# Performance work log

Hardware: AMD Instinct MI355X
Metric: run time of the kernel (lower is better)

## Reference

```python
import jax, jax.numpy as jnp
import numpy as np

NUM_LEVELS = 4
RADIUS = 4


def _avg_pool2(x):
    # F.avg_pool2d(x, 2, stride=2) for even H, W
    B, D, H, W = x.shape
    return x.reshape(B, D, H // 2, 2, W // 2, 2).mean(axis=(3, 5))


def _local_corr(f1, f2, coords, radius):
    # f1, f2: (B, D, H, W); coords: (B, 2, H, W) pixel coords into f2
    B, D, H, W = f1.shape
    offs = jnp.arange(-radius, radius + 1, dtype=coords.dtype)
    dx, dy = jnp.meshgrid(offs, offs, indexing='ij')  # x slow, y fast (as in _get_local_grids)
    dx = dx.reshape(-1)
    dy = dy.reshape(-1)  # (K,) with K=(2r+1)^2
    x = coords[:, 0][..., None] + dx  # (B,H,W,K)
    y = coords[:, 1][..., None] + dy
    # grid_sample(padding_mode='border', align_corners=True) == clamp coords then bilinear
    x = jnp.clip(x, 0.0, W - 1.0)
    y = jnp.clip(y, 0.0, H - 1.0)
    x0 = jnp.floor(x)
    y0 = jnp.floor(y)
    x1 = jnp.minimum(x0 + 1.0, W - 1.0)
    y1 = jnp.minimum(y0 + 1.0, H - 1.0)
    wx1 = x - x0
    wx0 = 1.0 - wx1
    wy1 = y - y0
    wy0 = 1.0 - wy1
    f2f = f2.reshape(B, D, H * W)

    def corner(xc, yc, w):
        idx = (yc * W + xc).astype(jnp.int32).reshape(B, -1)  # (B, H*W*K)
        g = jax.vmap(lambda f, i: jnp.take(f, i, axis=1))(f2f, idx)  # (B,D,H*W*K)
        g = g.reshape(B, D, H, W, -1)  # (B,D,H,W,K)
        # per-pixel dot over feature dim, weighted by bilinear weight
        return w * jnp.einsum('bdhw,bdhwk->bhwk', f1, g)

    corr = (corner(x0, y0, wx0 * wy0) + corner(x1, y0, wx1 * wy0)
            + corner(x0, y1, wx0 * wy1) + corner(x1, y1, wx1 * wy1))
    corr = corr / jnp.sqrt(jnp.asarray(D, dtype=corr.dtype))
    return jnp.transpose(corr, (0, 3, 1, 2))  # (B,K,H,W)


def _corr_pyramid(fmap1, fmap2, coords):
    p1, p2 = [fmap1], [fmap2]
    for _ in range(NUM_LEVELS - 1):
        p1.append(_avg_pool2(p1[-1]))
        p2.append(_avg_pool2(p2[-1]))
    outs = []
    B = coords.shape[0]
    for i in range(NUM_LEVELS):
        Hl, Wl = p1[i].shape[2], p1[i].shape[3]
        if i == 0:
            c = coords
        else:
            c = jax.image.resize(coords, (B, 2, Hl, Wl), method='linear')
        c = c / (2.0 ** i)  # coords / scale, per level
        outs.append(_local_corr(p1[i], p2[i], c, RADIUS))
    return tuple(outs)


def setup_inputs() -> dict:
    key = jax.random.key(0)
    k1, k2, k3 = jax.random.split(key, 3)
    B, D, H, W = 1, 128, 64, 96
    fmap1 = jax.random.normal(k1, (B, D, H, W), dtype=jnp.float32)
    fmap2 = jax.random.normal(k2, (B, D, H, W), dtype=jnp.float32)
    yy, xx = jnp.meshgrid(jnp.arange(H, dtype=jnp.float32),
                          jnp.arange(W, dtype=jnp.float32), indexing='ij')
    base = jnp.stack([xx, yy], axis=0)[None]  # (1,2,H,W), coords_grid order (x,y)
    flow = 3.0 * jax.random.normal(k3, (B, 2, H, W), dtype=jnp.float32)
    coords = base + flow
    return {"fmap1": fmap1, "fmap2": fmap2, "coords": coords}


def reference(fmap1, fmap2, coords):
    return _corr_pyramid(fmap1, fmap2, coords)
```

## Files before the change

kernel.cpp:

```cpp
#include <hip/hip_runtime.h>
#include <hip/hip_fp16.h>

#define D 128
#define H0 64
#define W0 96
#define HW0 6144
#define INV_SQRT_D 0.08838834764831843f

#define H_F1T0 0
#define H_F1T1 786432
#define H_F1T2 983040
#define H_F1T3 1032192
#define H_F2T0 1048576
#define H_F2T1 1835008
#define H_F2T2 2031616
#define H_F2T3 2080768

#define OUT_L0 0
#define OUT_L1 497664
#define OUT_L2 622080
#define OUT_L3 653184

typedef _Float16 h2 __attribute__((ext_vector_type(2)));
union F4H { float4 f; h2 h[4]; };

__device__ __forceinline__ float dot2f(h2 a, h2 b, float c) {
#if __has_builtin(__builtin_amdgcn_fdot2)
    return __builtin_amdgcn_fdot2(a, b, c, false);
#else
    return c + (float)a.x * (float)b.x + (float)a.y * (float)b.y;
#endif
}

__device__ __forceinline__ void gp_to_level(int gp, int& level, int& p) {
    if (gp < 6144)      { level = 0; p = gp; }
    else if (gp < 7680) { level = 1; p = gp - 6144; }
    else if (gp < 8064) { level = 2; p = gp - 7680; }
    else                { level = 3; p = gp - 8064; }
}

__global__ __launch_bounds__(256) void k_prep(const float* __restrict__ f1,
                                              const float* __restrict__ f2,
                                              float* __restrict__ ws) {
    const int b = blockIdx.x;
    const int t = threadIdx.x;
    _Float16* wh = (_Float16*)ws;
    __shared__ float T[64 * 69];
    const int m = b / 192;
    const int rb = b - m * 192;
    const int tix = rb >> 1;
    const int dh = rb & 1;
    const int tr = tix / 12, tc = tix - (tix / 12) * 12;
    const float* in = (m ? f2 : f1) + dh * 64 * HW0;

    const int l = t & 63;
    const int gbase = (tr * 8 + (l >> 3)) * W0 + tc * 8 + (l & 7);
#pragma unroll 4
    for (int pass = 0; pass < 16; ++pass) {
        int d = pass * 4 + (t >> 6);
        T[l * 69 + d] = in[d * HW0 + gbase];
    }
    __syncthreads();

    _Float16* o0 = wh + (m ? H_F2T0 : H_F1T0) + dh * 64;
#pragma unroll 4
    for (int pass = 0; pass < 16; ++pass) {
        int e = t + pass * 256;
        int pl = e >> 6, c = e & 63;
        int gp = (tr * 8 + (pl >> 3)) * W0 + tc * 8 + (pl & 7);
        o0[gp * D + c] = (_Float16)T[pl * 69 + c];
    }
    _Float16* o1 = wh + (m ? H_F2T1 : H_F1T1) + dh * 64;
#pragma unroll
    for (int pass = 0; pass < 4; ++pass) {
        int e = t + pass * 256;
        int d = e & 63, p1 = e >> 6;
        int i1 = p1 >> 2, j1 = p1 & 3;
        int l00 = (i1 * 2) * 8 + j1 * 2;
        float v = T[l00 * 69 + d] + T[(l00 + 1) * 69 + d]
                + T[(l00 + 8) * 69 + d] + T[(l00 + 9) * 69 + d];
        o1[((tr * 4 + i1) * 48 + tc * 4 + j1) * D + d] = (_Float16)(0.25f * v);
    }
    _Float16* o2 = wh + (m ? H_F2T2 : H_F1T2) + dh * 64;
    {
        int d = t & 63, p2 = t >> 6;
        int i2 = p2 >> 1, j2 = p2 & 1;
        float acc = 0.0f;
#pragma unroll
        for (int a = 0; a < 4; ++a)
#pragma unroll
            for (int c2 = 0; c2 < 4; ++c2)
                acc += T[((i2 * 4 + a) * 8 + j2 * 4 + c2) * 69 + d];
        o2[((tr * 2 + i2) * 24 + tc * 2 + j2) * D + d] = (_Float16)(acc * 0.0625f);
    }
    _Float16* o3 = wh + (m ? H_F2T3 : H_F1T3) + dh * 64;
    if (t < 64) {
        float acc = 0.0f;
        for (int l2 = 0; l2 < 64; ++l2) acc += T[l2 * 69 + t];
        o3[(tr * 12 + tc) * D + t] = (_Float16)(acc * 0.015625f);
    }
}

__global__ __launch_bounds__(1024) void k_dc(const float* __restrict__ coords0,
                                             const float* __restrict__ ws,
                                             float* __restrict__ out) {
    __shared__ float Gs[16 * 101];
    __shared__ float cxs[16], cys[16];
    const _Float16* wh = (const _Float16*)ws;

    const int t = threadIdx.x;
    const int w = t >> 6;
    const int ln = t & 63;
    const int oct = ln >> 3;
    const int sub = ln & 7;

    const int gp0 = blockIdx.x * 16;
    const int gp = gp0 + w;

    int level, p;
    gp_to_level(gp, level, p);
    const int Hl = H0 >> level, Wl = W0 >> level;

    const int f1offs[4] = {H_F1T0, H_F1T1, H_F1T2, H_F1T3};
    const int f2offs[4] = {H_F2T0, H_F2T1, H_F2T2, H_F2T3};
    const int outoffs[4] = {OUT_L0, OUT_L1, OUT_L2, OUT_L3};

    const _Float16* f2t = wh + f2offs[level];

    float cx, cy;
    if (level == 0) {
        cx = coords0[p];
        cy = coords0[HW0 + p];
    } else {
        const int ho = p / Wl, wo = p - (p / Wl) * Wl;
        const float ff = (float)(1 << level);
        const float sfy = (ho + 0.5f) * ff - 0.5f;
        const float sfx = (wo + 0.5f) * ff - 0.5f;
        int ylo = max(0, (int)ceilf(sfy - ff));
        int yhi = min(H0 - 1, (int)floorf(sfy + ff));
        int xlo = max(0, (int)ceilf(sfx - ff));
        int xhi = min(W0 - 1, (int)floorf(sfx + ff));
        int nx = xhi - xlo + 1;
        int nt = (yhi - ylo + 1) * nx;
        float a0 = 0.0f, a1 = 0.0f, wsum = 0.0f;
        for (int i = ln; i < nt; i += 64) {
            int ry = i / nx, rx = i - ry * nx;
            int iy = ylo + ry, ix = xlo + rx;
            float wy = fmaxf(1.0f - fabsf(sfy - (float)iy) / ff, 0.0f);
            float wx = fmaxf(1.0f - fabsf(sfx - (float)ix) / ff, 0.0f);
            float wgt = wy * wx;
            wsum += wgt;
            a0 += wgt * coords0[iy * W0 + ix];
            a1 += wgt * coords0[HW0 + iy * W0 + ix];
        }
#pragma unroll
        for (int off = 32; off; off >>= 1) {
            a0 += __shfl_xor(a0, off);
            a1 += __shfl_xor(a1, off);
            wsum += __shfl_xor(wsum, off);
        }
        cx = a0 / wsum / ff;
        cy = a1 / wsum / ff;
    }
    if (ln == 0) { cxs[w] = cx; cys[w] = cy; }
    const int fx = (int)floorf(cx), fy = (int)floorf(cy);

    const _Float16* f1p = wh + f1offs[level] + p * D + sub * 8;
    F4H a0f, a1f;
    a0f.f = *(const float4*)(f1p);
    a1f.f = *(const float4*)(f1p + 64);

#pragma unroll 2
    for (int i = 0; i < 13; ++i) {
        int g = i * 8 + oct;
        int gc = min(g, 99);
        int gy = gc / 10;
        int gx = gc - gy * 10;
        int iy = min(max(fy - 4 + gy, 0), Hl - 1);
        int ix = min(max(fx - 4 + gx, 0), Wl - 1);
        const _Float16* row = f2t + (iy * Wl + ix) * D + sub * 8;
        F4H v0, v1;
        v0.f = *(const float4*)(row);
        v1.f = *(const float4*)(row + 64);
        float s = 0.0f;
        s = dot2f(a0f.h[0], v0.h[0], s);
        s = dot2f(a0f.h[1], v0.h[1], s);
        s = dot2f(a0f.h[2], v0.h[2], s);
        s = dot2f(a0f.h[3], v0.h[3], s);
        s = dot2f(a1f.h[0], v1.h[0], s);
        s = dot2f(a1f.h[1], v1.h[1], s);
        s = dot2f(a1f.h[2], v1.h[2], s);
        s = dot2f(a1f.h[3], v1.h[3], s);
        s += __shfl_xor(s, 1);
        s += __shfl_xor(s, 2);
        s += __shfl_xor(s, 4);
        if (sub == 0 && g < 100) Gs[w * 101 + g] = s;
    }
    __syncthreads();

    {
        const int px = t & 15;
        const int kk = t >> 4;
        int lv0, p0;
        gp_to_level(gp0, lv0, p0);
        const int Hb = H0 >> lv0, Wb = W0 >> lv0;
        const int npb = Hb * Wb;
        float* outp = out + outoffs[lv0] + p0 + px;
        const float bx = cxs[px], by = cys[px];
        const float Wm1 = (float)(Wb - 1), Hm1 = (float)(Hb - 1);
        const float* Gp = &Gs[px * 101];

        for (int k = kk; k < 81; k += 64) {
            int dxi = k / 9, dyi = k - (k / 9) * 9;
            float x = fminf(fmaxf(bx + (float)(dxi - 4), 0.0f), Wm1);
            float y = fminf(fmaxf(by + (float)(dyi - 4), 0.0f), Hm1);
            float wx1 = x - floorf(x), wx0 = 1.0f - wx1;
            float wy1 = y - floorf(y), wy0 = 1.0f - wy1;
            int g00 = dyi * 10 + dxi;
            float v = wx0 * wy0 * Gp[g00]      + wx1 * wy0 * Gp[g00 + 1]
                    + wx0 * wy1 * Gp[g00 + 10] + wx1 * wy1 * Gp[g00 + 11];
            outp[k * npb] = v * INV_SQRT_D;
        }
    }
}

extern "C" void kernel_launch(void* const* d_in, const int* in_sizes, int n_in,
                              void* d_out, int out_size, void* d_ws, size_t ws_size,
                              hipStream_t stream) {
    const float* fmap1  = (const float*)d_in[0];
    const float* fmap2  = (const float*)d_in[1];
    const float* coords = (const float*)d_in[2];
    float* out = (float*)d_out;
    float* ws = (float*)d_ws;

    k_prep<<<dim3(384), dim3(256), 0, stream>>>(fmap1, fmap2, ws);
    k_dc<<<dim3(510), dim3(1024), 0, stream>>>(coords, ws, out);
}
```

Measured before the change: 79.21 us.

## Split prep into quarter-channel blocks with float4 loads and packed half2 stores

The feature transpose/pool kernel now runs 768 blocks of 512 threads, each handling 32 channels of an 8x8 tile. It loads with float4 and writes level-0 output as packed half2, which cuts the per-thread load loop and raises parallelism. In the correlation kernel, the f1 feature load is hoisted ahead of the coordinate computation to overlap latency. Divisions by 10 and 9 and the row multiply are replaced with multiply-shift arithmetic, and an occupancy hint is added to launch bounds. Smaller shared tiles and more blocks add per-block overhead and yield narrower level-1..3 writes.

```diff
diff --git a/kernel.cpp b/kernel.cpp
--- a/kernel.cpp
+++ b/kernel.cpp
@@ -39,71 +39,80 @@
     else                { level = 3; p = gp - 8064; }
 }
 
-__global__ __launch_bounds__(256) void k_prep(const float* __restrict__ f1,
+__global__ __launch_bounds__(512) void k_prep(const float* __restrict__ f1,
                                               const float* __restrict__ f2,
                                               float* __restrict__ ws) {
     const int b = blockIdx.x;
     const int t = threadIdx.x;
     _Float16* wh = (_Float16*)ws;
-    __shared__ float T[64 * 69];
-    const int m = b / 192;
-    const int rb = b - m * 192;
-    const int tix = rb >> 1;
-    const int dh = rb & 1;
+    __shared__ float T[64 * 33];
+    const int m  = b / 384;
+    const int r  = b - m * 384;
+    const int tix = r >> 2;
+    const int dq  = r & 3;
     const int tr = tix / 12, tc = tix - (tix / 12) * 12;
-    const float* in = (m ? f2 : f1) + dh * 64 * HW0;
-
-    const int l = t & 63;
-    const int gbase = (tr * 8 + (l >> 3)) * W0 + tc * 8 + (l & 7);
-#pragma unroll 4
-    for (int pass = 0; pass < 16; ++pass) {
-        int d = pass * 4 + (t >> 6);
-        T[l * 69 + d] = in[d * HW0 + gbase];
+    const float* in = (m ? f2 : f1) + dq * 32 * HW0;
+
+    {
+        const int dl  = t >> 4;
+        const int row = (t >> 1) & 7;
+        const int c4  = t & 1;
+        float4 v = *(const float4*)(in + dl * HW0 + (tr * 8 + row) * W0
+                                    + tc * 8 + c4 * 4);
+        const int l0 = row * 8 + c4 * 4;
+        T[(l0 + 0) * 33 + dl] = v.x;
+        T[(l0 + 1) * 33 + dl] = v.y;
+        T[(l0 + 2) * 33 + dl] = v.z;
+        T[(l0 + 3) * 33 + dl] = v.w;
     }
     __syncthreads();
 
-    _Float16* o0 = wh + (m ? H_F2T0 : H_F1T0) + dh * 64;
-#pragma unroll 4
-    for (int pass = 0; pass < 16; ++pass) {
-        int e = t + pass * 256;
-        int pl = e >> 6, c = e & 63;
-        int gp = (tr * 8 + (pl >> 3)) * W0 + tc * 8 + (pl & 7);
-        o0[gp * D + c] = (_Float16)T[pl * 69 + c];
-    }
-    _Float16* o1 = wh + (m ? H_F2T1 : H_F1T1) + dh * 64;
-#pragma unroll
-    for (int pass = 0; pass < 4; ++pass) {
-        int e = t + pass * 256;
-        int d = e & 63, p1 = e >> 6;
+    {
+        _Float16* o0 = wh + (m ? H_F2T0 : H_F1T0) + dq * 32;
+        h2* o0h = (h2*)o0;
+#pragma unroll
+        for (int pass = 0; pass < 2; ++pass) {
+            int idx = t + pass * 512;
+            int pl = idx >> 4, c2 = idx & 15;
+            h2 hv;
+            hv.x = (_Float16)T[pl * 33 + 2 * c2];
+            hv.y = (_Float16)T[pl * 33 + 2 * c2 + 1];
+            int gp = (tr * 8 + (pl >> 3)) * W0 + tc * 8 + (pl & 7);
+            o0h[gp * 64 + c2] = hv;
+        }
+    }
+    {
+        _Float16* o1 = wh + (m ? H_F2T1 : H_F1T1) + dq * 32;
+        int d = t & 31, p1 = t >> 5;
         int i1 = p1 >> 2, j1 = p1 & 3;
         int l00 = (i1 * 2) * 8 + j1 * 2;
-        float v = T[l00 * 69 + d] + T[(l00 + 1) * 69 + d]
-                + T[(l00 + 8) * 69 + d] + T[(l00 + 9) * 69 + d];
+        float v = T[l00 * 33 + d] + T[(l00 + 1) * 33 + d]
+                + T[(l00 + 8) * 33 + d] + T[(l00 + 9) * 33 + d];
         o1[((tr * 4 + i1) * 48 + tc * 4 + j1) * D + d] = (_Float16)(0.25f * v);
     }
-    _Float16* o2 = wh + (m ? H_F2T2 : H_F1T2) + dh * 64;
-    {
-        int d = t & 63, p2 = t >> 6;
+    if (t < 128) {
+        _Float16* o2 = wh + (m ? H_F2T2 : H_F1T2) + dq * 32;
+        int d = t & 31, p2 = t >> 5;
         int i2 = p2 >> 1, j2 = p2 & 1;
         float acc = 0.0f;
 #pragma unroll
         for (int a = 0; a < 4; ++a)
 #pragma unroll
             for (int c2 = 0; c2 < 4; ++c2)
-                acc += T[((i2 * 4 + a) * 8 + j2 * 4 + c2) * 69 + d];
+                acc += T[((i2 * 4 + a) * 8 + j2 * 4 + c2) * 33 + d];
         o2[((tr * 2 + i2) * 24 + tc * 2 + j2) * D + d] = (_Float16)(acc * 0.0625f);
     }
-    _Float16* o3 = wh + (m ? H_F2T3 : H_F1T3) + dh * 64;
-    if (t < 64) {
+    if (t < 32) {
+        _Float16* o3 = wh + (m ? H_F2T3 : H_F1T3) + dq * 32;
         float acc = 0.0f;
-        for (int l2 = 0; l2 < 64; ++l2) acc += T[l2 * 69 + t];
+        for (int l2 = 0; l2 < 64; ++l2) acc += T[l2 * 33 + t];
         o3[(tr * 12 + tc) * D + t] = (_Float16)(acc * 0.015625f);
     }
 }
 
-__global__ __launch_bounds__(1024) void k_dc(const float* __restrict__ coords0,
-                                             const float* __restrict__ ws,
-                                             float* __restrict__ out) {
+__global__ __launch_bounds__(1024, 8) void k_dc(const float* __restrict__ coords0,
+                                                const float* __restrict__ ws,
+                                                float* __restrict__ out) {
     __shared__ float Gs[16 * 101];
     __shared__ float cxs[16], cys[16];
     const _Float16* wh = (const _Float16*)ws;
@@ -126,6 +135,11 @@
     const int outoffs[4] = {OUT_L0, OUT_L1, OUT_L2, OUT_L3};
 
     const _Float16* f2t = wh + f2offs[level];
+
+    const _Float16* f1p = wh + f1offs[level] + p * D + sub * 8;
+    F4H a0f, a1f;
+    a0f.f = *(const float4*)(f1p);
+    a1f.f = *(const float4*)(f1p + 64);
 
     float cx, cy;
     if (level == 0) {
@@ -164,21 +178,18 @@
     }
     if (ln == 0) { cxs[w] = cx; cys[w] = cy; }
     const int fx = (int)floorf(cx), fy = (int)floorf(cy);
-
-    const _Float16* f1p = wh + f1offs[level] + p * D + sub * 8;
-    F4H a0f, a1f;
-    a0f.f = *(const float4*)(f1p);
-    a1f.f = *(const float4*)(f1p + 64);
+    const int shf = 5 - level;
 
 #pragma unroll 2
     for (int i = 0; i < 13; ++i) {
         int g = i * 8 + oct;
         int gc = min(g, 99);
-        int gy = gc / 10;
+        int gy = (gc * 205) >> 11;
         int gx = gc - gy * 10;
         int iy = min(max(fy - 4 + gy, 0), Hl - 1);
         int ix = min(max(fx - 4 + gx, 0), Wl - 1);
-        const _Float16* row = f2t + (iy * Wl + ix) * D + sub * 8;
+        int rowp = ((iy * 3) << shf) + ix;
+        const _Float16* row = f2t + rowp * D + sub * 8;
         F4H v0, v1;
         v0.f = *(const float4*)(row);
         v1.f = *(const float4*)(row + 64);
@@ -211,7 +222,8 @@
         const float* Gp = &Gs[px * 101];
 
         for (int k = kk; k < 81; k += 64) {
-            int dxi = k / 9, dyi = k - (k / 9) * 9;
+            int dxi = (k * 57) >> 9;
+            int dyi = k - dxi * 9;
             float x = fminf(fmaxf(bx + (float)(dxi - 4), 0.0f), Wm1);
             float y = fminf(fmaxf(by + (float)(dyi - 4), 0.0f), Hm1);
             float wx1 = x - floorf(x), wx0 = 1.0f - wx1;
@@ -233,6 +245,6 @@
     float* out = (float*)d_out;
     float* ws = (float*)d_ws;
 
-    k_prep<<<dim3(384), dim3(256), 0, stream>>>(fmap1, fmap2, ws);
+    k_prep<<<dim3(768), dim3(512), 0, stream>>>(fmap1, fmap2, ws);
     k_dc<<<dim3(510), dim3(1024), 0, stream>>>(coords, ws, out);
 }
```

After: 78.45 us. About the same (-1.0%).
